# Kernel optimization log

Measured on AMD Instinct MI355X. Metric: run time of the kernel, lower is better.

## Reference

```python
import jax, jax.numpy as jnp
import numpy as np


def setup_inputs() -> dict:
    key = jax.random.key(0)
    k1, k2, k3 = jax.random.split(key, 3)
    D, N, K = 512, 131072, 64
    x = jax.random.normal(k1, (D, N), dtype=jnp.float32)
    a_bar = jax.random.uniform(k2, (K, N), dtype=jnp.float32)
    c = jax.random.normal(k3, (K, D), dtype=jnp.float32)
    return {"x": x, "a_bar": a_bar, "c": c}


def reference(x, a_bar, c):
    # V[k, d] = sum_n a_bar[k, n] * (x[d, n] - c[k, d])
    #         = (a_bar @ x.T)[k, d] - c[k, d] * sum_n a_bar[k, n]
    # Fused form: one GEMM + one row-sum, never materializing (K, D, N) residuals.
    ax = jnp.einsum('kn,dn->kd', a_bar, x)        # (K, D)
    a_sum = jnp.sum(a_bar, axis=1, keepdims=True)  # (K, 1)
    V = ax - c * a_sum                              # (K, D)
    return V
```

## Files before the change

### kernel.cpp

```cpp
#include <hip/hip_runtime.h>
#include <hip/hip_bf16.h>


#define K_ROWS 64
#define D_COLS 512
#define N_RED  131072LL
#define TOTAL_STEPS 2048
#define XBY 16384
#define ABY 8192
#define BUFB (XBY + ABY)

typedef __attribute__((ext_vector_type(8))) short short8;
typedef __attribute__((ext_vector_type(4))) float f32x4;

static __device__ __forceinline__ short f2bf(float f) {
    __bf16 h = (__bf16)f;
    return __builtin_bit_cast(short, h);
}
static __device__ __forceinline__ float bf2f(unsigned short u) {
    return __builtin_bit_cast(float, (unsigned)u << 16);
}
static __device__ __forceinline__ short8 cvt8(float4 a, float4 b) {
    short8 r;
    r[0] = f2bf(a.x); r[1] = f2bf(a.y); r[2] = f2bf(a.z); r[3] = f2bf(a.w);
    r[4] = f2bf(b.x); r[5] = f2bf(b.y); r[6] = f2bf(b.z); r[7] = f2bf(b.w);
    return r;
}

__global__ __launch_bounds__(512, 6) void vlad_stage1(
    const float* __restrict__ x, const float* __restrict__ ab,
    unsigned short* __restrict__ pax, float* __restrict__ pasum, int S)
{
    __shared__ __align__(16) char smem[2][BUFB];

    const int bid = blockIdx.x;
    const int x7  = bid & 7;
    const int g   = (bid >> 3) & 3;
    const int m   = bid >> 5;
    const int s   = m * 8 + x7;
    const int tid = threadIdx.x;
    const int w   = tid >> 6, l = tid & 63, lr = l & 15, lg = l >> 4;
    const int d0  = g * 128;

    const int st0 = (int)(((long long)s       * TOTAL_STEPS) / S);
    const int st1 = (int)(((long long)(s + 1) * TOTAL_STEPS) / S);

    const int xrow = tid >> 2, xq = tid & 3;
    const float* gx = x + (size_t)(d0 + xrow) * N_RED + xq * 16;
    const int xo0 = xrow * 128 + (((xq * 2)     ^ (xrow & 7)) << 4);
    const int xo1 = xrow * 128 + (((xq * 2 + 1) ^ (xrow & 7)) << 4);
    const int arow = tid >> 3, aq = tid & 7;
    const float* ga = ab + (size_t)arow * N_RED + aq * 8;
    const int ao0 = XBY + arow * 128 + ((aq ^ (arow & 7)) << 4);

    const int swz = lr & 7;
    int fx[2], fa[4][2];
    #pragma unroll
    for (int kk = 0; kk < 2; ++kk) {
        fx[kk] = (w * 16 + lr) * 128 + ((((kk << 2) | lg) ^ swz) << 4);
        #pragma unroll
        for (int t = 0; t < 4; ++t)
            fa[t][kk] = XBY + (t * 16 + lr) * 128 + ((((kk << 2) | lg) ^ swz) << 4);
    }

    f32x4 acc[4] = {};
    float asum = 0.f;
    float4 X0, X1, X2, X3, A0, A1;

    auto issue = [&](int it) {
        const float* p = gx + (size_t)it * 64;
        X0 = *(const float4*)(p);
        X1 = *(const float4*)(p + 4);
        X2 = *(const float4*)(p + 8);
        X3 = *(const float4*)(p + 12);
        const float* q = ga + (size_t)it * 64;
        A0 = *(const float4*)(q);
        A1 = *(const float4*)(q + 4);
    };
    auto commit = [&](char* buf) {
        *(short8*)(buf + xo0) = cvt8(X0, X1);
        *(short8*)(buf + xo1) = cvt8(X2, X3);
        *(short8*)(buf + ao0) = cvt8(A0, A1);
        asum += ((A0.x + A0.y) + (A0.z + A0.w))
              + ((A1.x + A1.y) + (A1.z + A1.w));
    };

    issue(st0);
    commit(smem[0]);

    int cur = 0;
    #pragma unroll 1
    for (int it = st0; it < st1; ++it) {
        const bool more = (it + 1 < st1);
        __syncthreads();
        if (more) issue(it + 1);

        const char* b = smem[cur];
        #pragma unroll
        for (int kk = 0; kk < 2; ++kk) {
            short8 xf  = *(const short8*)(b + fx[kk]);
            short8 a0f = *(const short8*)(b + fa[0][kk]);
            short8 a1f = *(const short8*)(b + fa[1][kk]);
            short8 a2f = *(const short8*)(b + fa[2][kk]);
            short8 a3f = *(const short8*)(b + fa[3][kk]);
            acc[0] = __builtin_amdgcn_mfma_f32_16x16x32_bf16(a0f, xf, acc[0], 0, 0, 0);
            acc[1] = __builtin_amdgcn_mfma_f32_16x16x32_bf16(a1f, xf, acc[1], 0, 0, 0);
            acc[2] = __builtin_amdgcn_mfma_f32_16x16x32_bf16(a2f, xf, acc[2], 0, 0, 0);
            acc[3] = __builtin_amdgcn_mfma_f32_16x16x32_bf16(a3f, xf, acc[3], 0, 0, 0);
        }

        if (more) commit(smem[cur ^ 1]);
        cur ^= 1;
    }

    unsigned short* dst = pax + (size_t)s * (K_ROWS * D_COLS);
    #pragma unroll
    for (int t = 0; t < 4; ++t)
        #pragma unroll
        for (int r = 0; r < 4; ++r)
            dst[(((g * 8 + w) * 4 + t) * 4 + r) * 64 + l] =
                (unsigned short)f2bf(acc[t][r]);

    if (g == 0) {
        asum += __shfl_xor(asum, 1, 64);
        asum += __shfl_xor(asum, 2, 64);
        asum += __shfl_xor(asum, 4, 64);
        if ((tid & 7) == 0) pasum[s * K_ROWS + arow] = asum;
    }
}

__global__ __launch_bounds__(256) void vlad_stage2(
    const unsigned short* __restrict__ pax, const float* __restrict__ pasum,
    const float* __restrict__ c, float* __restrict__ out, int S)
{
    __shared__ float red[256];
    __shared__ float ared[256];
    const int t  = threadIdx.x;
    const int fo = t & 63;
    const int sp = t >> 6;
    const int fb = blockIdx.x * 64;
    const int f  = fb + fo;

    float acc = 0.f;
    for (int s = sp; s < S; s += 4)
        acc += bf2f(pax[(size_t)s * (K_ROWS * D_COLS) + f]);
    red[t] = acc;

    const int R = (fb >> 6) & 3, T = (fb >> 8) & 3;
    const int ka = T * 16 + (t & 3) * 4 + R;
    float pa = 0.f;
    for (int s2 = t >> 2; s2 < S; s2 += 64)
        pa += pasum[s2 * K_ROWS + ka];
    ared[t] = pa;
    __syncthreads();

    for (int st = 128; st >= 4; st >>= 1) {
        if (t < st) ared[t] += ared[t + st];
        __syncthreads();
    }
    if (sp == 0) {
        const int lr = f & 15, lg = (f >> 4) & 3;
        const int r  = (f >> 6) & 3, tt = (f >> 8) & 3;
        const int w  = (f >> 10) & 7, gg = (f >> 13) & 3;
        const int k  = tt * 16 + lg * 4 + r;
        const int d  = gg * 128 + w * 16 + lr;
        float v = red[t] + red[t + 64] + red[t + 128] + red[t + 192];
        out[k * D_COLS + d] = v - c[k * D_COLS + d] * ared[lg];
    }
}

extern "C" void kernel_launch(void* const* d_in, const int* in_sizes, int n_in,
                              void* d_out, int out_size, void* d_ws, size_t ws_size,
                              hipStream_t stream)
{
    const float* x  = (const float*)d_in[0];
    const float* ab = (const float*)d_in[1];
    const float* c  = (const float*)d_in[2];
    float* out = (float*)d_out;

    int S = 192;
    while (S > 24 &&
           (size_t)S * ((size_t)K_ROWS * D_COLS * 2 + K_ROWS * 4) > ws_size)
        S >>= 1;

    unsigned short* pax = (unsigned short*)d_ws;
    float* pasum = (float*)((char*)d_ws + (size_t)S * K_ROWS * D_COLS * 2);

    vlad_stage1<<<dim3(4 * S), dim3(512), 0, stream>>>(x, ab, pax, pasum, S);
    vlad_stage2<<<dim3((K_ROWS * D_COLS) / 64), dim3(256), 0, stream>>>(pax, pasum, c, out, S);
}
```

Before: 83.88 us.

## Widen D tile to 256 per block and halve K-step depth per stage

Each stage-1 block now covers 256 D columns instead of 128, with two D sub-tiles per wave sharing the same a_bar fragments. The per-step reduction depth drops from 64 to 32, which doubles the step count and shrinks the LDS tile. The point is to halve redundant a_bar reads across D groups and to raise MFMA reuse per LDS load. The split count S rises to 256 and the occupancy hint drops to 4 blocks. The trade-off is more accumulators per thread, more loop iterations with syncs, and a larger partial buffer for stage 2 to reduce.

```diff
diff --git a/kernel.cpp b/kernel.cpp
--- a/kernel.cpp
+++ b/kernel.cpp
@@ -5,12 +5,13 @@
 #define K_ROWS 64
 #define D_COLS 512
 #define N_RED  131072LL
-#define TOTAL_STEPS 2048
+#define TOTAL_STEPS 4096
 #define XBY 16384
-#define ABY 8192
+#define ABY 4096
 #define BUFB (XBY + ABY)
 
 typedef __attribute__((ext_vector_type(8))) short short8;
+typedef __attribute__((ext_vector_type(4))) short short4v;
 typedef __attribute__((ext_vector_type(4))) float f32x4;
 
 static __device__ __forceinline__ short f2bf(float f) {
@@ -26,8 +27,13 @@
     r[4] = f2bf(b.x); r[5] = f2bf(b.y); r[6] = f2bf(b.z); r[7] = f2bf(b.w);
     return r;
 }
+static __device__ __forceinline__ short4v cvt4(float4 a) {
+    short4v r;
+    r[0] = f2bf(a.x); r[1] = f2bf(a.y); r[2] = f2bf(a.z); r[3] = f2bf(a.w);
+    return r;
+}
 
-__global__ __launch_bounds__(512, 6) void vlad_stage1(
+__global__ __launch_bounds__(512, 4) void vlad_stage1(
     const float* __restrict__ x, const float* __restrict__ ab,
     unsigned short* __restrict__ pax, float* __restrict__ pasum, int S)
 {
@@ -35,54 +41,50 @@
 
     const int bid = blockIdx.x;
     const int x7  = bid & 7;
-    const int g   = (bid >> 3) & 3;
-    const int m   = bid >> 5;
+    const int g   = (bid >> 3) & 1;
+    const int m   = bid >> 4;
     const int s   = m * 8 + x7;
     const int tid = threadIdx.x;
     const int w   = tid >> 6, l = tid & 63, lr = l & 15, lg = l >> 4;
-    const int d0  = g * 128;
+    const int d0  = g * 256;
 
     const int st0 = (int)(((long long)s       * TOTAL_STEPS) / S);
     const int st1 = (int)(((long long)(s + 1) * TOTAL_STEPS) / S);
 
-    const int xrow = tid >> 2, xq = tid & 3;
-    const float* gx = x + (size_t)(d0 + xrow) * N_RED + xq * 16;
-    const int xo0 = xrow * 128 + (((xq * 2)     ^ (xrow & 7)) << 4);
-    const int xo1 = xrow * 128 + (((xq * 2 + 1) ^ (xrow & 7)) << 4);
+    const int xrow = tid >> 1, xh = tid & 1;
+    const float* gx = x + (size_t)(d0 + xrow) * N_RED + xh * 16;
+    const int xo0 = xrow * 64 + (((xh * 2)     ^ (xrow & 3)) << 4);
+    const int xo1 = xrow * 64 + (((xh * 2 + 1) ^ (xrow & 3)) << 4);
     const int arow = tid >> 3, aq = tid & 7;
-    const float* ga = ab + (size_t)arow * N_RED + aq * 8;
-    const int ao0 = XBY + arow * 128 + ((aq ^ (arow & 7)) << 4);
+    const float* ga = ab + (size_t)arow * N_RED + aq * 4;
+    const int ao0 = XBY + arow * 64 + (((aq >> 1) ^ (arow & 3)) << 4) + (aq & 1) * 8;
 
-    const int swz = lr & 7;
-    int fx[2], fa[4][2];
+    const int swz = lr & 3;
+    int fx[2], fa[4];
     #pragma unroll
-    for (int kk = 0; kk < 2; ++kk) {
-        fx[kk] = (w * 16 + lr) * 128 + ((((kk << 2) | lg) ^ swz) << 4);
-        #pragma unroll
-        for (int t = 0; t < 4; ++t)
-            fa[t][kk] = XBY + (t * 16 + lr) * 128 + ((((kk << 2) | lg) ^ swz) << 4);
-    }
+    for (int sub = 0; sub < 2; ++sub)
+        fx[sub] = (w * 32 + sub * 16 + lr) * 64 + ((lg ^ swz) << 4);
+    #pragma unroll
+    for (int t = 0; t < 4; ++t)
+        fa[t] = XBY + (t * 16 + lr) * 64 + ((lg ^ swz) << 4);
 
-    f32x4 acc[4] = {};
+    f32x4 acc[4][2] = {};
     float asum = 0.f;
-    float4 X0, X1, X2, X3, A0, A1;
+    float4 X0, X1, X2, X3, A0;
 
     auto issue = [&](int it) {
-        const float* p = gx + (size_t)it * 64;
+        const float* p = gx + (size_t)it * 32;
         X0 = *(const float4*)(p);
         X1 = *(const float4*)(p + 4);
         X2 = *(const float4*)(p + 8);
         X3 = *(const float4*)(p + 12);
-        const float* q = ga + (size_t)it * 64;
-        A0 = *(const float4*)(q);
-        A1 = *(const float4*)(q + 4);
+        A0 = *(const float4*)(ga + (size_t)it * 32);
     };
     auto commit = [&](char* buf) {
-        *(short8*)(buf + xo0) = cvt8(X0, X1);
-        *(short8*)(buf + xo1) = cvt8(X2, X3);
-        *(short8*)(buf + ao0) = cvt8(A0, A1);
-        asum += ((A0.x + A0.y) + (A0.z + A0.w))
-              + ((A1.x + A1.y) + (A1.z + A1.w));
+        *(short8*)(buf + xo0)  = cvt8(X0, X1);
+        *(short8*)(buf + xo1)  = cvt8(X2, X3);
+        *(short4v*)(buf + ao0) = cvt4(A0);
+        asum += (A0.x + A0.y) + (A0.z + A0.w);
     };
 
     issue(st0);
@@ -96,18 +98,20 @@
         if (more) issue(it + 1);
 
         const char* b = smem[cur];
-        #pragma unroll
-        for (int kk = 0; kk < 2; ++kk) {
-            short8 xf  = *(const short8*)(b + fx[kk]);
-            short8 a0f = *(const short8*)(b + fa[0][kk]);
-            short8 a1f = *(const short8*)(b + fa[1][kk]);
-            short8 a2f = *(const short8*)(b + fa[2][kk]);
-            short8 a3f = *(const short8*)(b + fa[3][kk]);
-            acc[0] = __builtin_amdgcn_mfma_f32_16x16x32_bf16(a0f, xf, acc[0], 0, 0, 0);
-            acc[1] = __builtin_amdgcn_mfma_f32_16x16x32_bf16(a1f, xf, acc[1], 0, 0, 0);
-            acc[2] = __builtin_amdgcn_mfma_f32_16x16x32_bf16(a2f, xf, acc[2], 0, 0, 0);
-            acc[3] = __builtin_amdgcn_mfma_f32_16x16x32_bf16(a3f, xf, acc[3], 0, 0, 0);
-        }
+        short8 xf0 = *(const short8*)(b + fx[0]);
+        short8 xf1 = *(const short8*)(b + fx[1]);
+        short8 a0f = *(const short8*)(b + fa[0]);
+        short8 a1f = *(const short8*)(b + fa[1]);
+        short8 a2f = *(const short8*)(b + fa[2]);
+        short8 a3f = *(const short8*)(b + fa[3]);
+        acc[0][0] = __builtin_amdgcn_mfma_f32_16x16x32_bf16(a0f, xf0, acc[0][0], 0, 0, 0);
+        acc[1][0] = __builtin_amdgcn_mfma_f32_16x16x32_bf16(a1f, xf0, acc[1][0], 0, 0, 0);
+        acc[2][0] = __builtin_amdgcn_mfma_f32_16x16x32_bf16(a2f, xf0, acc[2][0], 0, 0, 0);
+        acc[3][0] = __builtin_amdgcn_mfma_f32_16x16x32_bf16(a3f, xf0, acc[3][0], 0, 0, 0);
+        acc[0][1] = __builtin_amdgcn_mfma_f32_16x16x32_bf16(a0f, xf1, acc[0][1], 0, 0, 0);
+        acc[1][1] = __builtin_amdgcn_mfma_f32_16x16x32_bf16(a1f, xf1, acc[1][1], 0, 0, 0);
+        acc[2][1] = __builtin_amdgcn_mfma_f32_16x16x32_bf16(a2f, xf1, acc[2][1], 0, 0, 0);
+        acc[3][1] = __builtin_amdgcn_mfma_f32_16x16x32_bf16(a3f, xf1, acc[3][1], 0, 0, 0);
 
         if (more) commit(smem[cur ^ 1]);
         cur ^= 1;
@@ -117,15 +121,17 @@
     #pragma unroll
     for (int t = 0; t < 4; ++t)
         #pragma unroll
-        for (int r = 0; r < 4; ++r)
-            dst[(((g * 8 + w) * 4 + t) * 4 + r) * 64 + l] =
-                (unsigned short)f2bf(acc[t][r]);
+        for (int sub = 0; sub < 2; ++sub)
+            #pragma unroll
+            for (int r = 0; r < 4; ++r)
+                dst[(((((g * 8 + w) * 4 + t) * 2 + sub) * 4 + r)) * 64 + l] =
+                    (unsigned short)f2bf(acc[t][sub][r]);
 
     if (g == 0) {
         asum += __shfl_xor(asum, 1, 64);
         asum += __shfl_xor(asum, 2, 64);
         asum += __shfl_xor(asum, 4, 64);
-        if ((tid & 7) == 0) pasum[s * K_ROWS + arow] = asum;
+        if (aq == 0) pasum[s * K_ROWS + arow] = asum;
     }
 }
 
@@ -146,7 +152,7 @@
         acc += bf2f(pax[(size_t)s * (K_ROWS * D_COLS) + f]);
     red[t] = acc;
 
-    const int R = (fb >> 6) & 3, T = (fb >> 8) & 3;
+    const int R = (fb >> 6) & 3, T = (fb >> 9) & 3;
     const int ka = T * 16 + (t & 3) * 4 + R;
     float pa = 0.f;
     for (int s2 = t >> 2; s2 < S; s2 += 64)
@@ -160,10 +166,10 @@
     }
     if (sp == 0) {
         const int lr = f & 15, lg = (f >> 4) & 3;
-        const int r  = (f >> 6) & 3, tt = (f >> 8) & 3;
-        const int w  = (f >> 10) & 7, gg = (f >> 13) & 3;
+        const int r  = (f >> 6) & 3, sub = (f >> 8) & 1;
+        const int tt = (f >> 9) & 3, w = (f >> 11) & 7, gg = (f >> 14) & 1;
         const int k  = tt * 16 + lg * 4 + r;
-        const int d  = gg * 128 + w * 16 + lr;
+        const int d  = gg * 256 + w * 32 + sub * 16 + lr;
         float v = red[t] + red[t + 64] + red[t + 128] + red[t + 192];
         out[k * D_COLS + d] = v - c[k * D_COLS + d] * ared[lg];
     }
@@ -178,14 +184,14 @@
     const float* c  = (const float*)d_in[2];
     float* out = (float*)d_out;
 
-    int S = 192;
-    while (S > 24 &&
+    int S = 256;
+    while (S > 32 &&
            (size_t)S * ((size_t)K_ROWS * D_COLS * 2 + K_ROWS * 4) > ws_size)
         S >>= 1;
 
     unsigned short* pax = (unsigned short*)d_ws;
     float* pasum = (float*)((char*)d_ws + (size_t)S * K_ROWS * D_COLS * 2);
 
-    vlad_stage1<<<dim3(4 * S), dim3(512), 0, stream>>>(x, ab, pax, pasum, S);
+    vlad_stage1<<<dim3(2 * S), dim3(512), 0, stream>>>(x, ab, pax, pasum, S);
     vlad_stage2<<<dim3((K_ROWS * D_COLS) / 64), dim3(256), 0, stream>>>(pax, pasum, c, out, S);
 }
```

Result: faster. 77.96 us (-7.1%).

## Shrink stage1 tiles to 64 D-columns and 32-wide K steps with 256-thread blocks

Applied to the files above, without the earlier changes.

Stage1 blocks now cover 64 columns of D instead of 128 and use 256 threads, with a 32-element reduction step per iteration instead of 64. The grid doubles to 8*S blocks and LDS per buffer drops from 24KB to 8KB, which is meant to raise occupancy and spread the load across CUs. In exchange the a_bar tile is re-read by twice as many D-groups, so global traffic for a_bar doubles, and each iteration pays more sync overhead per unit of MFMA work. Stage2's index decoding is updated to match the new layout of the partial sums.

```diff
diff --git a/kernel.cpp b/kernel.cpp
--- a/kernel.cpp
+++ b/kernel.cpp
@@ -5,9 +5,9 @@
 #define K_ROWS 64
 #define D_COLS 512
 #define N_RED  131072LL
-#define TOTAL_STEPS 2048
-#define XBY 16384
-#define ABY 8192
+#define TOTAL_STEPS 4096
+#define XBY 4096
+#define ABY 4096
 #define BUFB (XBY + ABY)
 
 typedef __attribute__((ext_vector_type(8))) short short8;
@@ -27,7 +27,7 @@
     return r;
 }
 
-__global__ __launch_bounds__(512, 6) void vlad_stage1(
+__global__ __launch_bounds__(256, 6) void vlad_stage1(
     const float* __restrict__ x, const float* __restrict__ ab,
     unsigned short* __restrict__ pax, float* __restrict__ pasum, int S)
 {
@@ -35,52 +35,44 @@
 
     const int bid = blockIdx.x;
     const int x7  = bid & 7;
-    const int g   = (bid >> 3) & 3;
-    const int m   = bid >> 5;
+    const int g   = (bid >> 3) & 7;
+    const int m   = bid >> 6;
     const int s   = m * 8 + x7;
     const int tid = threadIdx.x;
     const int w   = tid >> 6, l = tid & 63, lr = l & 15, lg = l >> 4;
-    const int d0  = g * 128;
+    const int d0  = g * 64;
 
     const int st0 = (int)(((long long)s       * TOTAL_STEPS) / S);
     const int st1 = (int)(((long long)(s + 1) * TOTAL_STEPS) / S);
 
-    const int xrow = tid >> 2, xq = tid & 3;
-    const float* gx = x + (size_t)(d0 + xrow) * N_RED + xq * 16;
-    const int xo0 = xrow * 128 + (((xq * 2)     ^ (xrow & 7)) << 4);
-    const int xo1 = xrow * 128 + (((xq * 2 + 1) ^ (xrow & 7)) << 4);
-    const int arow = tid >> 3, aq = tid & 7;
-    const float* ga = ab + (size_t)arow * N_RED + aq * 8;
-    const int ao0 = XBY + arow * 128 + ((aq ^ (arow & 7)) << 4);
+    const int row = tid >> 2, q = tid & 3;
+    const float* gx = x  + (size_t)(d0 + row) * N_RED + q * 8;
+    const float* ga = ab + (size_t)row        * N_RED + q * 8;
+    const int xo = row * 64 + ((q ^ (row & 3)) << 4);
+    const int ao = XBY + xo;
 
-    const int swz = lr & 7;
-    int fx[2], fa[4][2];
+    const int swz = lr & 3;
+    const int fx = (w * 16 + lr) * 64 + ((lg ^ swz) << 4);
+    int fa[4];
     #pragma unroll
-    for (int kk = 0; kk < 2; ++kk) {
-        fx[kk] = (w * 16 + lr) * 128 + ((((kk << 2) | lg) ^ swz) << 4);
-        #pragma unroll
-        for (int t = 0; t < 4; ++t)
-            fa[t][kk] = XBY + (t * 16 + lr) * 128 + ((((kk << 2) | lg) ^ swz) << 4);
-    }
+    for (int t = 0; t < 4; ++t)
+        fa[t] = XBY + (t * 16 + lr) * 64 + ((lg ^ swz) << 4);
 
     f32x4 acc[4] = {};
     float asum = 0.f;
-    float4 X0, X1, X2, X3, A0, A1;
+    float4 X0, X1, A0, A1;
 
     auto issue = [&](int it) {
-        const float* p = gx + (size_t)it * 64;
+        const float* p = gx + (size_t)it * 32;
         X0 = *(const float4*)(p);
         X1 = *(const float4*)(p + 4);
-        X2 = *(const float4*)(p + 8);
-        X3 = *(const float4*)(p + 12);
-        const float* q = ga + (size_t)it * 64;
-        A0 = *(const float4*)(q);
-        A1 = *(const float4*)(q + 4);
+        const float* qq = ga + (size_t)it * 32;
+        A0 = *(const float4*)(qq);
+        A1 = *(const float4*)(qq + 4);
     };
     auto commit = [&](char* buf) {
-        *(short8*)(buf + xo0) = cvt8(X0, X1);
-        *(short8*)(buf + xo1) = cvt8(X2, X3);
-        *(short8*)(buf + ao0) = cvt8(A0, A1);
+        *(short8*)(buf + xo) = cvt8(X0, X1);
+        *(short8*)(buf + ao) = cvt8(A0, A1);
         asum += ((A0.x + A0.y) + (A0.z + A0.w))
               + ((A1.x + A1.y) + (A1.z + A1.w));
     };
@@ -96,18 +88,15 @@
         if (more) issue(it + 1);
 
         const char* b = smem[cur];
-        #pragma unroll
-        for (int kk = 0; kk < 2; ++kk) {
-            short8 xf  = *(const short8*)(b + fx[kk]);
-            short8 a0f = *(const short8*)(b + fa[0][kk]);
-            short8 a1f = *(const short8*)(b + fa[1][kk]);
-            short8 a2f = *(const short8*)(b + fa[2][kk]);
-            short8 a3f = *(const short8*)(b + fa[3][kk]);
-            acc[0] = __builtin_amdgcn_mfma_f32_16x16x32_bf16(a0f, xf, acc[0], 0, 0, 0);
-            acc[1] = __builtin_amdgcn_mfma_f32_16x16x32_bf16(a1f, xf, acc[1], 0, 0, 0);
-            acc[2] = __builtin_amdgcn_mfma_f32_16x16x32_bf16(a2f, xf, acc[2], 0, 0, 0);
-            acc[3] = __builtin_amdgcn_mfma_f32_16x16x32_bf16(a3f, xf, acc[3], 0, 0, 0);
-        }
+        short8 xf  = *(const short8*)(b + fx);
+        short8 a0f = *(const short8*)(b + fa[0]);
+        short8 a1f = *(const short8*)(b + fa[1]);
+        short8 a2f = *(const short8*)(b + fa[2]);
+        short8 a3f = *(const short8*)(b + fa[3]);
+        acc[0] = __builtin_amdgcn_mfma_f32_16x16x32_bf16(a0f, xf, acc[0], 0, 0, 0);
+        acc[1] = __builtin_amdgcn_mfma_f32_16x16x32_bf16(a1f, xf, acc[1], 0, 0, 0);
+        acc[2] = __builtin_amdgcn_mfma_f32_16x16x32_bf16(a2f, xf, acc[2], 0, 0, 0);
+        acc[3] = __builtin_amdgcn_mfma_f32_16x16x32_bf16(a3f, xf, acc[3], 0, 0, 0);
 
         if (more) commit(smem[cur ^ 1]);
         cur ^= 1;
@@ -118,14 +107,13 @@
     for (int t = 0; t < 4; ++t)
         #pragma unroll
         for (int r = 0; r < 4; ++r)
-            dst[(((g * 8 + w) * 4 + t) * 4 + r) * 64 + l] =
+            dst[(((g * 4 + w) * 4 + t) * 4 + r) * 64 + l] =
                 (unsigned short)f2bf(acc[t][r]);
 
     if (g == 0) {
         asum += __shfl_xor(asum, 1, 64);
         asum += __shfl_xor(asum, 2, 64);
-        asum += __shfl_xor(asum, 4, 64);
-        if ((tid & 7) == 0) pasum[s * K_ROWS + arow] = asum;
+        if (q == 0) pasum[s * K_ROWS + row] = asum;
     }
 }
 
@@ -161,9 +149,9 @@
     if (sp == 0) {
         const int lr = f & 15, lg = (f >> 4) & 3;
         const int r  = (f >> 6) & 3, tt = (f >> 8) & 3;
-        const int w  = (f >> 10) & 7, gg = (f >> 13) & 3;
+        const int w  = (f >> 10) & 3, gg = (f >> 12) & 7;
         const int k  = tt * 16 + lg * 4 + r;
-        const int d  = gg * 128 + w * 16 + lr;
+        const int d  = gg * 64 + w * 16 + lr;
         float v = red[t] + red[t + 64] + red[t + 128] + red[t + 192];
         out[k * D_COLS + d] = v - c[k * D_COLS + d] * ared[lg];
     }
@@ -186,6 +174,6 @@
     unsigned short* pax = (unsigned short*)d_ws;
     float* pasum = (float*)((char*)d_ws + (size_t)S * K_ROWS * D_COLS * 2);
 
-    vlad_stage1<<<dim3(4 * S), dim3(512), 0, stream>>>(x, ab, pax, pasum, S);
+    vlad_stage1<<<dim3(8 * S), dim3(256), 0, stream>>>(x, ab, pax, pasum, S);
     vlad_stage2<<<dim3((K_ROWS * D_COLS) / 64), dim3(256), 0, stream>>>(pax, pasum, c, out, S);
 }
```

Measured after the change: 77.93 us. -7.1%, faster.
